# Performance work log

Measured on AMD Instinct MI355X. Metric: run time of the kernel, lower is better.

The kernel has to match this reference:

```python
import jax, jax.numpy as jnp
import numpy as np

N_NODES = 4096
N_EDGES = 131072
F_DIM = 16
H_DIM = 32

def _mlp_params(key, in_dim, hidden):
    ks = jax.random.split(key, 6)
    s1 = 1.0 / np.sqrt(in_dim); s2 = 1.0 / np.sqrt(hidden)
    return dict(
        W1=jax.random.uniform(ks[0], (in_dim, hidden), jnp.float32, -s1, s1),
        b1=jax.random.uniform(ks[1], (hidden,), jnp.float32, -s1, s1),
        W2=jax.random.uniform(ks[2], (hidden, hidden), jnp.float32, -s2, s2),
        b2=jax.random.uniform(ks[3], (hidden,), jnp.float32, -s2, s2),
        W3=jax.random.uniform(ks[4], (hidden, 1), jnp.float32, -s2, s2),
        b3=jax.random.uniform(ks[5], (1,), jnp.float32, -s2, s2),
    )

def _mlp(x, W1, b1, W2, b2, W3, b3):
    h = jax.nn.relu(x @ W1 + b1)
    h = jax.nn.relu(h @ W2 + b2)
    return (h @ W3 + b3)[..., 0]  # (E,)

def setup_inputs() -> dict:
    key = jax.random.key(0)
    k_ei, k_ef, k_s, k_p = jax.random.split(key, 4)
    edge_index = jax.random.randint(k_ei, (N_EDGES, 2), 0, N_NODES, dtype=jnp.int32)
    edge_feat = jax.random.normal(k_ef, (N_EDGES, F_DIM), dtype=jnp.float32)
    sh = _mlp_params(k_s, F_DIM, H_DIM)
    sp = _mlp_params(k_p, F_DIM, H_DIM)
    return dict(
        species_idx=0,
        edge_index=edge_index,
        edge_feat=edge_feat,
        num_nodes=N_NODES,
        sW1=sh['W1'], sb1=sh['b1'], sW2=sh['W2'], sb2=sh['b2'], sW3=sh['W3'], sb3=sh['b3'],
        pW1=sp['W1'], pb1=sp['b1'], pW2=sp['W2'], pb2=sp['b2'], pW3=sp['W3'], pb3=sp['b3'],
    )

def reference(species_idx, edge_index, edge_feat, num_nodes,
              sW1, sb1, sW2, sb2, sW3, sb3,
              pW1, pb1, pW2, pb2, pW3, pb3):
    # Edge logits: shared head + species head (species_idx selects the head;
    # here the selected head's params are passed directly).
    shared = _mlp(edge_feat, sW1, sb1, sW2, sb2, sW3, sb3)   # (E,)
    species = _mlp(edge_feat, pW1, pb1, pW2, pb2, pW3, pb3)  # (E,)
    resistance = jax.nn.softplus(shared + species) + 1e-4
    conductance = 1.0 / resistance
    i = edge_index[:, 0]
    j = edge_index[:, 1]
    # Scatter-assembled graph Laplacian (N x N)
    L = jnp.zeros((num_nodes, num_nodes), dtype=edge_feat.dtype)
    L = L.at[i, i].add(conductance)
    L = L.at[j, j].add(conductance)
    L = L.at[i, j].add(-conductance)
    L = L.at[j, i].add(-conductance)
    L_pinv = jnp.linalg.pinv(L)
    diag = jnp.diagonal(L_pinv)
    R = diag[:, None] + diag[None, :] - 2.0 * L_pinv
    return R, shared, species
```

## Files before the change

kernel.cpp:

```cpp
#include <hip/hip_runtime.h>
#include <hip/hip_bf16.h>


#define NN 4096
#define LDA 4096
#define NEDGE 131072
#define INVN (1.0f/4096.0f)

__device__ __forceinline__ float mlp_eval(const float* __restrict__ w,
                                          const float* __restrict__ x) {
  float h1[32], h2[32];
#pragma unroll
  for (int o = 0; o < 32; o += 4) {
    float4 s = *(const float4*)&w[512 + o];
#pragma unroll
    for (int i = 0; i < 16; ++i) {
      float4 wv = *(const float4*)&w[i * 32 + o];
      s.x = fmaf(x[i], wv.x, s.x); s.y = fmaf(x[i], wv.y, s.y);
      s.z = fmaf(x[i], wv.z, s.z); s.w = fmaf(x[i], wv.w, s.w);
    }
    h1[o] = fmaxf(s.x, 0.f); h1[o+1] = fmaxf(s.y, 0.f);
    h1[o+2] = fmaxf(s.z, 0.f); h1[o+3] = fmaxf(s.w, 0.f);
  }
#pragma unroll
  for (int o = 0; o < 32; o += 4) {
    float4 s = *(const float4*)&w[1568 + o];
#pragma unroll
    for (int i = 0; i < 32; ++i) {
      float4 wv = *(const float4*)&w[544 + i * 32 + o];
      s.x = fmaf(h1[i], wv.x, s.x); s.y = fmaf(h1[i], wv.y, s.y);
      s.z = fmaf(h1[i], wv.z, s.z); s.w = fmaf(h1[i], wv.w, s.w);
    }
    h2[o] = fmaxf(s.x, 0.f); h2[o+1] = fmaxf(s.y, 0.f);
    h2[o+2] = fmaxf(s.z, 0.f); h2[o+3] = fmaxf(s.w, 0.f);
  }
  float out = w[1632];
#pragma unroll
  for (int i = 0; i < 32; ++i) out = fmaf(h2[i], w[1600 + i], out);
  return out;
}

__global__ __launch_bounds__(256) void mlp_kernel(
    const float* __restrict__ ef,
    const float* __restrict__ sW1, const float* __restrict__ sb1,
    const float* __restrict__ sW2, const float* __restrict__ sb2,
    const float* __restrict__ sW3, const float* __restrict__ sb3,
    const float* __restrict__ pW1, const float* __restrict__ pb1,
    const float* __restrict__ pW2, const float* __restrict__ pb2,
    const float* __restrict__ pW3, const float* __restrict__ pb3,
    float* __restrict__ outS, float* __restrict__ outP,
    float* __restrict__ cond) {
  __shared__ float w[3328];
  int t = threadIdx.x;
  for (int i = t; i < 512; i += 256) { w[i] = sW1[i]; w[1664 + i] = pW1[i]; }
  for (int i = t; i < 1024; i += 256) { w[544 + i] = sW2[i]; w[1664 + 544 + i] = pW2[i]; }
  if (t < 32) {
    w[512 + t] = sb1[t]; w[1568 + t] = sb2[t]; w[1600 + t] = sW3[t];
    w[1664 + 512 + t] = pb1[t]; w[1664 + 1568 + t] = pb2[t]; w[1664 + 1600 + t] = pW3[t];
  }
  if (t == 0) { w[1632] = sb3[0]; w[1664 + 1632] = pb3[0]; }
  __syncthreads();
  int e = blockIdx.x * 256 + t;
  float x[16];
#pragma unroll
  for (int i = 0; i < 16; i += 4) {
    float4 v = *(const float4*)&ef[(size_t)e * 16 + i];
    x[i] = v.x; x[i+1] = v.y; x[i+2] = v.z; x[i+3] = v.w;
  }
  float s = mlp_eval(w, x);
  float p = mlp_eval(w + 1664, x);
  outS[e] = s; outP[e] = p;
  float z = s + p;
  float sp = fmaxf(z, 0.f) + log1pf(expf(-fabsf(z)));
  cond[e] = 1.0f / (sp + 1e-4f);
}

__global__ __launch_bounds__(256) void init_A(float* __restrict__ A) {
  size_t q = (size_t)blockIdx.x * 256 + threadIdx.x;
  *(float4*)&A[q * 4] = make_float4(INVN, INVN, INVN, INVN);
}

__global__ __launch_bounds__(256) void scatter_kernel(const int* __restrict__ ei,
                                                      const float* __restrict__ cond,
                                                      float* __restrict__ A) {
  int e = blockIdx.x * 256 + threadIdx.x;
  int i = ei[2 * e], j = ei[2 * e + 1];
  float c = cond[e];
  atomicAdd(&A[(size_t)i * (LDA + 1)], c);
  atomicAdd(&A[(size_t)j * (LDA + 1)], c);
  atomicAdd(&A[(size_t)i * LDA + j], -c);
  atomicAdd(&A[(size_t)j * LDA + i], -c);
}

__device__ __forceinline__ float rlane(float v, int l) {
  return __int_as_float(__builtin_amdgcn_readlane(__float_as_int(v), l));
}

__global__ __launch_bounds__(64) void potf2_wave(float* __restrict__ A, int k,
                                                 float* __restrict__ GinvAll) {
  float* blk = A + (size_t)k * 64 * (LDA + 1);
  const int lane = threadIdx.x;
  float a[64], x[64];
#pragma unroll
  for (int c = 0; c < 64; c += 4) {
    float4 v = *(const float4*)&blk[(size_t)lane * LDA + c];
    a[c] = v.x; a[c+1] = v.y; a[c+2] = v.z; a[c+3] = v.w;
    x[c]   = (c   == lane) ? 1.f : 0.f;
    x[c+1] = (c+1 == lane) ? 1.f : 0.f;
    x[c+2] = (c+2 == lane) ? 1.f : 0.f;
    x[c+3] = (c+3 == lane) ? 1.f : 0.f;
  }
#pragma unroll
  for (int j = 0; j < 64; ++j) {
    float dj = rlane(a[j], j);
    float inv = 1.0f / sqrtf(dj);
    float lij = a[j] * inv;
    a[j] = lij;
    float coefT = -lij;
    float sX = (lane == j) ? inv : 1.0f;
    float coefX = (lane > j) ? -lij : 0.0f;
#pragma unroll
    for (int c = j + 1; c < 64; ++c)
      a[c] = fmaf(coefT, rlane(lij, c), a[c]);
#pragma unroll
    for (int c = 0; c <= j; ++c) {
      float xjc = rlane(x[c], j) * inv;
      x[c] = fmaf(coefX, xjc, x[c] * sX);
    }
  }
  float* Gk = GinvAll + (size_t)k * 4096;
#pragma unroll
  for (int c = 0; c < 64; c += 4) {
    *(float4*)&blk[(size_t)lane * LDA + c] = make_float4(a[c], a[c+1], a[c+2], a[c+3]);
    *(float4*)&Gk[lane * 64 + c] = make_float4(x[c], x[c+1], x[c+2], x[c+3]);
  }
}

template <bool TA, bool TB, bool ACCUM, bool LOWER, bool KST, bool CCOMP>
__global__ __launch_bounds__(256) void gemm64(
    const float* __restrict__ Ab, long long aZ, int lda,
    const float* __restrict__ Bb, long long bZ, int ldb,
    float* __restrict__ Cb, long long cZ, int ldc, int K, float alpha) {
  int ti = blockIdx.x, tj = blockIdx.y;
  if (LOWER && tj > ti) return;
  const float* A = Ab + (long long)blockIdx.z * aZ;
  const float* B = Bb + (long long)blockIdx.z * bZ;
  __shared__ float As[16][68], Bs[16][68];
  int tid = threadIdx.x;
  int tx = tid & 15, ty = tid >> 4;
  float acc[4][4] = {};
  int m0 = ti * 64, n0 = tj * 64;
  int k0 = KST ? ti * 64 : 0;
  for (int k = k0; k < K; k += 16) {
    if (!TA) {
      int r = tid >> 2, c4 = (tid & 3) * 4;
      float4 v = *(const float4*)&A[(size_t)(m0 + r) * lda + k + c4];
      As[c4 + 0][r] = v.x; As[c4 + 1][r] = v.y; As[c4 + 2][r] = v.z; As[c4 + 3][r] = v.w;
    } else {
      int r = tid >> 4, c4 = (tid & 15) * 4;
      *(float4*)&As[r][c4] = *(const float4*)&A[(size_t)(k + r) * lda + m0 + c4];
    }
    if (TB) {
      int r = tid >> 2, c4 = (tid & 3) * 4;
      float4 v = *(const float4*)&B[(size_t)(n0 + r) * ldb + k + c4];
      Bs[c4 + 0][r] = v.x; Bs[c4 + 1][r] = v.y; Bs[c4 + 2][r] = v.z; Bs[c4 + 3][r] = v.w;
    } else {
      int r = tid >> 4, c4 = (tid & 15) * 4;
      *(float4*)&Bs[r][c4] = *(const float4*)&B[(size_t)(k + r) * ldb + n0 + c4];
    }
    __syncthreads();
#pragma unroll
    for (int kk = 0; kk < 16; ++kk) {
      float4 av = *(const float4*)&As[kk][ty * 4];
      float4 bv = *(const float4*)&Bs[kk][tx * 4];
      float a[4] = {av.x, av.y, av.z, av.w};
      float b[4] = {bv.x, bv.y, bv.z, bv.w};
#pragma unroll
      for (int i = 0; i < 4; ++i)
#pragma unroll
        for (int jj = 0; jj < 4; ++jj) acc[i][jj] = fmaf(a[i], b[jj], acc[i][jj]);
    }
    __syncthreads();
  }
  if (CCOMP) {
    float* C = Cb + ((size_t)ti * (ti + 1) / 2 + tj) * 4096;
#pragma unroll
    for (int i = 0; i < 4; ++i) {
      float4 c;
      c.x = alpha * acc[i][0]; c.y = alpha * acc[i][1];
      c.z = alpha * acc[i][2]; c.w = alpha * acc[i][3];
      *(float4*)&C[(ty * 4 + i) * 64 + tx * 4] = c;
    }
  } else {
    float* C = Cb + (long long)blockIdx.z * cZ;
#pragma unroll
    for (int i = 0; i < 4; ++i) {
      size_t off = (size_t)(m0 + ty * 4 + i) * ldc + n0 + tx * 4;
      float4 c;
      if (ACCUM) {
        c = *(float4*)&C[off];
        c.x += alpha * acc[i][0]; c.y += alpha * acc[i][1];
        c.z += alpha * acc[i][2]; c.w += alpha * acc[i][3];
      } else {
        c.x = alpha * acc[i][0]; c.y = alpha * acc[i][1];
        c.z = alpha * acc[i][2]; c.w = alpha * acc[i][3];
      }
      *(float4*)&C[off] = c;
    }
  }
}

template <bool TA, bool TB, bool ACCUM, bool TRI, bool KST, bool CCOMP>
__global__ __launch_bounds__(256) void gemm128(
    const float* __restrict__ Ab, long long aZ, int lda,
    const float* __restrict__ Bb, long long bZ, int ldb,
    float* __restrict__ Cb, long long cZ, int ldc, int K, float alpha) {
  int ti, tj;
  if (TRI) {
    int bid = blockIdx.x;
    ti = (int)((sqrtf(8.0f * bid + 1.0f) - 1.0f) * 0.5f);
    while ((ti + 1) * (ti + 2) / 2 <= bid) ++ti;
    while (ti * (ti + 1) / 2 > bid) --ti;
    tj = bid - ti * (ti + 1) / 2;
  } else {
    ti = blockIdx.x; tj = blockIdx.y;
  }
  const float* A = Ab + (long long)blockIdx.z * aZ;
  const float* B = Bb + (long long)blockIdx.z * bZ;
  __shared__ float As[16][132], Bs[16][132];
  int tid = threadIdx.x;
  int tx = tid & 15, ty = tid >> 4;
  float acc[8][8] = {};
  int m0 = ti * 128, n0 = tj * 128;
  int k0 = KST ? ti * 128 : 0;
  for (int k = k0; k < K; k += 16) {
    if (!TA) {
      int r = tid >> 1, c8 = (tid & 1) * 8;
      const float* src = &A[(size_t)(m0 + r) * lda + k + c8];
      float4 v0 = *(const float4*)src;
      float4 v1 = *(const float4*)(src + 4);
      As[c8 + 0][r] = v0.x; As[c8 + 1][r] = v0.y; As[c8 + 2][r] = v0.z; As[c8 + 3][r] = v0.w;
      As[c8 + 4][r] = v1.x; As[c8 + 5][r] = v1.y; As[c8 + 6][r] = v1.z; As[c8 + 7][r] = v1.w;
    } else {
      int r = tid >> 4, c8 = (tid & 15) * 8;
      const float* src = &A[(size_t)(k + r) * lda + m0 + c8];
      *(float4*)&As[r][c8]     = *(const float4*)src;
      *(float4*)&As[r][c8 + 4] = *(const float4*)(src + 4);
    }
    if (TB) {
      int r = tid >> 1, c8 = (tid & 1) * 8;
      const float* src = &B[(size_t)(n0 + r) * ldb + k + c8];
      float4 v0 = *(const float4*)src;
      float4 v1 = *(const float4*)(src + 4);
      Bs[c8 + 0][r] = v0.x; Bs[c8 + 1][r] = v0.y; Bs[c8 + 2][r] = v0.z; Bs[c8 + 3][r] = v0.w;
      Bs[c8 + 4][r] = v1.x; Bs[c8 + 5][r] = v1.y; Bs[c8 + 6][r] = v1.z; Bs[c8 + 7][r] = v1.w;
    } else {
      int r = tid >> 4, c8 = (tid & 15) * 8;
      const float* src = &B[(size_t)(k + r) * ldb + n0 + c8];
      *(float4*)&Bs[r][c8]     = *(const float4*)src;
      *(float4*)&Bs[r][c8 + 4] = *(const float4*)(src + 4);
    }
    __syncthreads();
#pragma unroll
    for (int kk = 0; kk < 16; ++kk) {
      float a8[8], b8[8];
      *(float4*)&a8[0] = *(const float4*)&As[kk][ty * 4];
      *(float4*)&a8[4] = *(const float4*)&As[kk][64 + ty * 4];
      *(float4*)&b8[0] = *(const float4*)&Bs[kk][tx * 4];
      *(float4*)&b8[4] = *(const float4*)&Bs[kk][64 + tx * 4];
#pragma unroll
      for (int i = 0; i < 8; ++i)
#pragma unroll
        for (int jj = 0; jj < 8; ++jj) acc[i][jj] = fmaf(a8[i], b8[jj], acc[i][jj]);
    }
    __syncthreads();
  }
  if (CCOMP) {
#pragma unroll
    for (int hr = 0; hr < 2; ++hr) {
      int TI = 2 * ti + hr;
#pragma unroll
      for (int hc = 0; hc < 2; ++hc) {
        int TJ = 2 * tj + hc;
        if (TJ > TI) continue;
        float* C = Cb + ((size_t)TI * (TI + 1) / 2 + TJ) * 4096;
#pragma unroll
        for (int i = 0; i < 4; ++i) {
          float4 c;
          c.x = alpha * acc[hr * 4 + i][hc * 4 + 0];
          c.y = alpha * acc[hr * 4 + i][hc * 4 + 1];
          c.z = alpha * acc[hr * 4 + i][hc * 4 + 2];
          c.w = alpha * acc[hr * 4 + i][hc * 4 + 3];
          *(float4*)&C[(ty * 4 + i) * 64 + tx * 4] = c;
        }
      }
    }
  } else {
    float* C = Cb + (long long)blockIdx.z * cZ;
#pragma unroll
    for (int i = 0; i < 8; ++i) {
      int row = (i < 4) ? (m0 + ty * 4 + i) : (m0 + 64 + ty * 4 + i - 4);
      float* dst0 = &C[(size_t)row * ldc + n0 + tx * 4];
      float* dst1 = dst0 + 64;
      float4 c0, c1;
      c0.x = alpha * acc[i][0]; c0.y = alpha * acc[i][1];
      c0.z = alpha * acc[i][2]; c0.w = alpha * acc[i][3];
      c1.x = alpha * acc[i][4]; c1.y = alpha * acc[i][5];
      c1.z = alpha * acc[i][6]; c1.w = alpha * acc[i][7];
      if (ACCUM) {
        float4 o0 = *(float4*)dst0, o1 = *(float4*)dst1;
        c0.x += o0.x; c0.y += o0.y; c0.z += o0.z; c0.w += o0.w;
        c1.x += o1.x; c1.y += o1.y; c1.z += o1.z; c1.w += o1.w;
      }
      *(float4*)dst0 = c0;
      *(float4*)dst1 = c1;
    }
  }
}

__global__ __launch_bounds__(256) void finish_W_prep(float* __restrict__ A,
                                                     const float* __restrict__ GinvAll) {
  size_t q = (size_t)blockIdx.x * 256 + threadIdx.x;
  int r = (int)(q >> 10), c4 = (int)(q & 1023) << 2;
  int rb = r >> 6, cb = c4 >> 6;
  if (cb == rb) {
    const float* g = GinvAll + (size_t)rb * 4096 + (size_t)(r & 63) * 64 + (c4 & 63);
    *(float4*)&A[q * 4] = *(const float4*)g;
  } else if (cb > rb) {
    *(float4*)&A[q * 4] = make_float4(0.f, 0.f, 0.f, 0.f);
  }
}

__global__ __launch_bounds__(256) void copy_diag(const float* __restrict__ Mc,
                                                 float* __restrict__ d) {
  int i = blockIdx.x * 256 + threadIdx.x;
  int tb = i >> 6;
  size_t q = (size_t)tb * (tb + 1) / 2 + tb;
  d[i] = Mc[q * 4096 + (size_t)(i & 63) * 65];
}

__global__ __launch_bounds__(256) void final_R(const float* __restrict__ Mc,
                                               const float* __restrict__ d,
                                               float* __restrict__ out) {
  size_t idx = (size_t)blockIdx.x * 256 + threadIdx.x;
  int r = (int)(idx >> 12), c = (int)(idx & 4095);
  int a = r > c ? r : c, b = r > c ? c : r;
  int ta = a >> 6, tb = b >> 6;
  size_t q = (size_t)ta * (ta + 1) / 2 + tb;
  float m = Mc[q * 4096 + (size_t)(a & 63) * 64 + (b & 63)];
  out[idx] = d[r] + d[c] - 2.0f * m;
}

extern "C" void kernel_launch(void* const* d_in, const int* in_sizes, int n_in,
                              void* d_out, int out_size, void* d_ws, size_t ws_size,
                              hipStream_t stream) {
  const int* eidx = (const int*)d_in[1];
  const float* ef = (const float*)d_in[2];
  const float* sW1 = (const float*)d_in[4],  *sb1 = (const float*)d_in[5];
  const float* sW2 = (const float*)d_in[6],  *sb2 = (const float*)d_in[7];
  const float* sW3 = (const float*)d_in[8],  *sb3 = (const float*)d_in[9];
  const float* pW1 = (const float*)d_in[10], *pb1 = (const float*)d_in[11];
  const float* pW2 = (const float*)d_in[12], *pb2 = (const float*)d_in[13];
  const float* pW3 = (const float*)d_in[14], *pb3 = (const float*)d_in[15];

  float* dout = (float*)d_out;
  float* dA = dout;
  float* outS = dout + (size_t)NN * NN;
  float* outP = outS + NEDGE;

  float* ws = (float*)d_ws;
  float* Mc = ws;
  float* U = ws + 8519680ull;
  float* cond = U;
  float* Ginv = U;
  float* Tbuf = U;
  float* diagb = U;

  mlp_kernel<<<NEDGE / 256, 256, 0, stream>>>(ef, sW1, sb1, sW2, sb2, sW3, sb3,
                                              pW1, pb1, pW2, pb2, pW3, pb3,
                                              outS, outP, cond);
  init_A<<<(NN * NN / 4) / 256, 256, 0, stream>>>(dA);
  scatter_kernel<<<NEDGE / 256, 256, 0, stream>>>(eidx, cond, dA);

  for (int p = 0; p < 16; ++p) {
    int ct = p * 4;
    for (int kk = 0; kk < 4; ++kk) {
      int k = ct + kk;
      potf2_wave<<<1, 64, 0, stream>>>(dA, k, Ginv);
      int rem = NN - (k + 1) * 64;
      if (rem > 0) {
        float* panel = dA + (size_t)(k + 1) * 64 * LDA + (size_t)k * 64;
        gemm64<false, true, false, false, false, false>
            <<<dim3(rem / 64, 1, 1), 256, 0, stream>>>(
                panel, 0, LDA, Ginv + (size_t)k * 4096, 0, 64, panel, 0, LDA,
                64, 1.0f);
        int pcols = 3 - kk;
        if (pcols > 0) {
          float* trail = dA + (size_t)(k + 1) * 64 * (LDA + 1);
          gemm64<false, true, true, true, false, false>
              <<<dim3(rem / 64, pcols, 1), 256, 0, stream>>>(
                  panel, 0, LDA, panel, 0, LDA, trail, 0, LDA, 64, -1.0f);
        }
      }
    }
    int c0 = p * 256;
    int rem2 = NN - c0 - 256;
    if (rem2 > 0) {
      float* Lp = dA + (size_t)(c0 + 256) * LDA + c0;
      float* trail = dA + (size_t)(c0 + 256) * (LDA + 1);
      int nt = rem2 / 128;
      gemm128<false, true, true, true, false, false>
          <<<dim3(nt * (nt + 1) / 2, 1, 1), 256, 0, stream>>>(
              Lp, 0, LDA, Lp, 0, LDA, trail, 0, LDA, 256, -1.0f);
    }
  }

  finish_W_prep<<<(NN * NN / 4) / 256, 256, 0, stream>>>(dA, Ginv);

  for (int S = 64; S <= 2048; S *= 2) {
    int np = NN / (2 * S);
    long long pz = (long long)2 * S * (LDA + 1);
    if (S == 64) {
      gemm64<false, false, false, false, false, false>
          <<<dim3(1, 1, np), 256, 0, stream>>>(
              dA + (size_t)S * LDA, pz, LDA, dA, pz, LDA,
              Tbuf, (long long)S * S, S, S, 1.0f);
      gemm64<false, false, false, false, false, false>
          <<<dim3(1, 1, np), 256, 0, stream>>>(
              dA + (size_t)S * (LDA + 1), pz, LDA, Tbuf, (long long)S * S, S,
              dA + (size_t)S * LDA, pz, LDA, S, -1.0f);
    } else {
      gemm128<false, false, false, false, false, false>
          <<<dim3(S / 128, S / 128, np), 256, 0, stream>>>(
              dA + (size_t)S * LDA, pz, LDA, dA, pz, LDA,
              Tbuf, (long long)S * S, S, S, 1.0f);
      gemm128<false, false, false, false, false, false>
          <<<dim3(S / 128, S / 128, np), 256, 0, stream>>>(
              dA + (size_t)S * (LDA + 1), pz, LDA, Tbuf, (long long)S * S, S,
              dA + (size_t)S * LDA, pz, LDA, S, -1.0f);
    }
  }

  gemm128<true, false, false, true, true, true>
      <<<dim3(528, 1, 1), 256, 0, stream>>>(dA, 0, LDA, dA, 0, LDA, Mc, 0, 64,
                                            NN, 1.0f);

  copy_diag<<<NN / 256, 256, 0, stream>>>(Mc, diagb);
  final_R<<<(NN * NN) / 256, 256, 0, stream>>>(Mc, diagb, dout);
}
```

Measured before the change: 5.171 ms.

## Fuse 256-wide diagonal Cholesky into one kernel, add fused panel TRSM and K-split Gram GEMM

Replaces the per-64-column sequence of potf2, panel GEMM and small SYRK launches with a single 512-thread kernel that factors each 256x256 diagonal block in shared memory. A new trsm_panel256 kernel then solves the whole 256-wide panel per 64-row block. The final triangular Gram GEMM is split along K into two halves that accumulate with atomics into a zeroed workspace, which doubles parallelism for the imbalanced KST launch. The aim is to cut the many tiny serial launches on the critical path, at the cost of running diagonal work on a single block and paying for atomic accumulation.

```diff
diff --git a/kernel.cpp b/kernel.cpp
--- a/kernel.cpp
+++ b/kernel.cpp
@@ -80,6 +80,11 @@
   *(float4*)&A[q * 4] = make_float4(INVN, INVN, INVN, INVN);
 }
 
+__global__ __launch_bounds__(256) void zero_ws(float* __restrict__ P) {
+  size_t q = (size_t)blockIdx.x * 256 + threadIdx.x;
+  *(float4*)&P[q * 4] = make_float4(0.f, 0.f, 0.f, 0.f);
+}
+
 __global__ __launch_bounds__(256) void scatter_kernel(const int* __restrict__ ei,
                                                       const float* __restrict__ cond,
                                                       float* __restrict__ A) {
@@ -96,10 +101,9 @@
   return __int_as_float(__builtin_amdgcn_readlane(__float_as_int(v), l));
 }
 
-__global__ __launch_bounds__(64) void potf2_wave(float* __restrict__ A, int k,
-                                                 float* __restrict__ GinvAll) {
-  float* blk = A + (size_t)k * 64 * (LDA + 1);
-  const int lane = threadIdx.x;
+__device__ __noinline__ void potf2_dev(float* __restrict__ A, int kt, int lane,
+                                       float (* __restrict__ GT)[68]) {
+  float* blk = A + (size_t)kt * 64 * (LDA + 1);
   float a[64], x[64];
 #pragma unroll
   for (int c = 0; c < 64; c += 4) {
@@ -128,11 +132,206 @@
       x[c] = fmaf(coefX, xjc, x[c] * sX);
     }
   }
-  float* Gk = GinvAll + (size_t)k * 4096;
-#pragma unroll
-  for (int c = 0; c < 64; c += 4) {
+#pragma unroll
+  for (int c = 0; c < 64; c += 4)
     *(float4*)&blk[(size_t)lane * LDA + c] = make_float4(a[c], a[c+1], a[c+2], a[c+3]);
-    *(float4*)&Gk[lane * 64 + c] = make_float4(x[c], x[c+1], x[c+2], x[c+3]);
+#pragma unroll
+  for (int c = 0; c < 64; ++c) GT[c][lane] = x[c];
+}
+
+__device__ __forceinline__ void syrk_tile(float* __restrict__ A, int t0, int ti_, int tj_,
+                                          const float (* __restrict__ LtA)[68],
+                                          const float (* __restrict__ LtB)[68], int gtid) {
+  int tx = gtid & 15, ty = gtid >> 4;
+  float acc[4][4] = {};
+  for (int k = 0; k < 64; ++k) {
+    float4 a4 = *(const float4*)&LtA[k][ty * 4];
+    float4 b4 = *(const float4*)&LtB[k][tx * 4];
+    float aa[4] = {a4.x, a4.y, a4.z, a4.w};
+    float bb[4] = {b4.x, b4.y, b4.z, b4.w};
+#pragma unroll
+    for (int i = 0; i < 4; ++i)
+#pragma unroll
+      for (int jj = 0; jj < 4; ++jj) acc[i][jj] = fmaf(aa[i], bb[jj], acc[i][jj]);
+  }
+  float* C = A + ((size_t)(t0 + ti_) * 64) * LDA + (size_t)(t0 + tj_) * 64;
+#pragma unroll
+  for (int i = 0; i < 4; ++i) {
+    float* p = &C[(size_t)(ty * 4 + i) * LDA + tx * 4];
+    float4 c = *(float4*)p;
+    c.x -= acc[i][0]; c.y -= acc[i][1]; c.z -= acc[i][2]; c.w -= acc[i][3];
+    *(float4*)p = c;
+  }
+}
+
+__global__ __launch_bounds__(512) void potrf_diag256(float* __restrict__ A,
+                                                     float* __restrict__ GinvAll,
+                                                     int p) {
+  __shared__ float GT[64][68];
+  __shared__ float At[2][64][68];
+  __shared__ float Lt[3][64][68];
+  int tid = threadIdx.x;
+  int wid = tid >> 6, lane = tid & 63;
+  int grp = tid >> 8, gtid = tid & 255;
+  int t0 = p * 4;
+  for (int kk = 0; kk < 4; ++kk) {
+    if (wid == 0) {
+      potf2_dev(A, t0 + kk, lane, GT);
+    } else if (grp == 1) {
+      const int TI_[5] = {2, 3, 2, 3, 3};
+      const int TJ_[5] = {1, 1, 2, 2, 3};
+#pragma unroll 5
+      for (int t = 0; t < 5; ++t) {
+        bool on = (kk == 1) || (kk == 2 && t >= 3);
+        if (on)
+          syrk_tile(A, t0, TI_[t], TJ_[t], Lt[TI_[t] - kk], Lt[TJ_[t] - kk], gtid);
+      }
+    }
+    __syncthreads();
+    {
+      int base = (t0 + kk) * 4096;
+#pragma unroll 8
+      for (int u = 0; u < 8; ++u) {
+        int q = tid * 8 + u;
+        GinvAll[base + q] = GT[q & 63][q >> 6];
+      }
+    }
+    for (int rnd = 0; rnd < 2; ++rnd) {
+      int it = kk + 1 + rnd * 2 + grp;
+      bool act = (it <= 3);
+      if (act) {
+        for (int q = gtid; q < 1024; q += 256) {
+          int r = q >> 4, k4 = (q & 15) << 2;
+          float4 v = *(const float4*)&A[((size_t)(t0 + it) * 64 + r) * LDA +
+                                        (size_t)(t0 + kk) * 64 + k4];
+          At[grp][k4 + 0][r] = v.x; At[grp][k4 + 1][r] = v.y;
+          At[grp][k4 + 2][r] = v.z; At[grp][k4 + 3][r] = v.w;
+        }
+      }
+      __syncthreads();
+      if (act) {
+        int tx = gtid & 15, ty = gtid >> 4;
+        float acc[4][4] = {};
+        for (int k = 0; k < 64; ++k) {
+          float4 a4 = *(const float4*)&At[grp][k][ty * 4];
+          float4 b4 = *(const float4*)&GT[k][tx * 4];
+          float aa[4] = {a4.x, a4.y, a4.z, a4.w};
+          float bb[4] = {b4.x, b4.y, b4.z, b4.w};
+#pragma unroll
+          for (int i = 0; i < 4; ++i)
+#pragma unroll
+            for (int jj = 0; jj < 4; ++jj) acc[i][jj] = fmaf(aa[i], bb[jj], acc[i][jj]);
+        }
+        int s = it - kk - 1;
+#pragma unroll
+        for (int jj = 0; jj < 4; ++jj)
+          *(float4*)&Lt[s][tx * 4 + jj][ty * 4] =
+              make_float4(acc[0][jj], acc[1][jj], acc[2][jj], acc[3][jj]);
+        float* C = A + ((size_t)(t0 + it) * 64) * LDA + (size_t)(t0 + kk) * 64;
+#pragma unroll
+        for (int i = 0; i < 4; ++i)
+          *(float4*)&C[(size_t)(ty * 4 + i) * LDA + tx * 4] =
+              make_float4(acc[i][0], acc[i][1], acc[i][2], acc[i][3]);
+      }
+      __syncthreads();
+    }
+    if (kk < 3 && grp == 0)
+      syrk_tile(A, t0, kk + 1, kk + 1, Lt[0], Lt[0], gtid);
+    __syncthreads();
+  }
+}
+
+__global__ __launch_bounds__(256) void trsm_panel256(float* __restrict__ A,
+                                                     const float* __restrict__ GinvAll,
+                                                     int p) {
+  __shared__ float Sr[64][260];
+  __shared__ float Bt[64][68];
+  int tid = threadIdx.x;
+  int c0 = p * 256;
+  int r0 = c0 + 256 + blockIdx.x * 64;
+  for (int q = tid; q < 4096; q += 256) {
+    int r = q >> 6, c4 = (q & 63) << 2;
+    *(float4*)&Sr[r][c4] = *(const float4*)&A[(size_t)(r0 + r) * LDA + c0 + c4];
+  }
+  __syncthreads();
+  int tx = tid & 15, ty = tid >> 4;
+  for (int j = 0; j < 4; ++j) {
+    float acc2[4][4] = {};
+    for (int p2 = 0; p2 < j; ++p2) {
+      for (int q = tid; q < 1024; q += 256) {
+        int c = q >> 4, k4 = (q & 15) << 2;
+        float4 v = *(const float4*)&A[(size_t)(c0 + j * 64 + c) * LDA +
+                                      c0 + p2 * 64 + k4];
+        Bt[k4 + 0][c] = v.x; Bt[k4 + 1][c] = v.y;
+        Bt[k4 + 2][c] = v.z; Bt[k4 + 3][c] = v.w;
+      }
+      __syncthreads();
+      for (int k = 0; k < 64; ++k) {
+        float a0 = Sr[ty * 4 + 0][p2 * 64 + k];
+        float a1 = Sr[ty * 4 + 1][p2 * 64 + k];
+        float a2 = Sr[ty * 4 + 2][p2 * 64 + k];
+        float a3 = Sr[ty * 4 + 3][p2 * 64 + k];
+        float4 b = *(const float4*)&Bt[k][tx * 4];
+        acc2[0][0] = fmaf(a0, b.x, acc2[0][0]); acc2[0][1] = fmaf(a0, b.y, acc2[0][1]);
+        acc2[0][2] = fmaf(a0, b.z, acc2[0][2]); acc2[0][3] = fmaf(a0, b.w, acc2[0][3]);
+        acc2[1][0] = fmaf(a1, b.x, acc2[1][0]); acc2[1][1] = fmaf(a1, b.y, acc2[1][1]);
+        acc2[1][2] = fmaf(a1, b.z, acc2[1][2]); acc2[1][3] = fmaf(a1, b.w, acc2[1][3]);
+        acc2[2][0] = fmaf(a2, b.x, acc2[2][0]); acc2[2][1] = fmaf(a2, b.y, acc2[2][1]);
+        acc2[2][2] = fmaf(a2, b.z, acc2[2][2]); acc2[2][3] = fmaf(a2, b.w, acc2[2][3]);
+        acc2[3][0] = fmaf(a3, b.x, acc2[3][0]); acc2[3][1] = fmaf(a3, b.y, acc2[3][1]);
+        acc2[3][2] = fmaf(a3, b.z, acc2[3][2]); acc2[3][3] = fmaf(a3, b.w, acc2[3][3]);
+      }
+      __syncthreads();
+    }
+    if (j > 0) {
+#pragma unroll
+      for (int i = 0; i < 4; ++i) {
+        Sr[ty * 4 + i][j * 64 + tx * 4 + 0] -= acc2[i][0];
+        Sr[ty * 4 + i][j * 64 + tx * 4 + 1] -= acc2[i][1];
+        Sr[ty * 4 + i][j * 64 + tx * 4 + 2] -= acc2[i][2];
+        Sr[ty * 4 + i][j * 64 + tx * 4 + 3] -= acc2[i][3];
+      }
+    }
+    __syncthreads();
+    {
+      const float* G = GinvAll + (size_t)(p * 4 + j) * 4096;
+      for (int q = tid; q < 1024; q += 256) {
+        int c = q >> 4, k4 = (q & 15) << 2;
+        float4 v = *(const float4*)&G[c * 64 + k4];
+        Bt[k4 + 0][c] = v.x; Bt[k4 + 1][c] = v.y;
+        Bt[k4 + 2][c] = v.z; Bt[k4 + 3][c] = v.w;
+      }
+    }
+    __syncthreads();
+    float acc3[4][4] = {};
+    for (int k = 0; k < 64; ++k) {
+      float a0 = Sr[ty * 4 + 0][j * 64 + k];
+      float a1 = Sr[ty * 4 + 1][j * 64 + k];
+      float a2 = Sr[ty * 4 + 2][j * 64 + k];
+      float a3 = Sr[ty * 4 + 3][j * 64 + k];
+      float4 b = *(const float4*)&Bt[k][tx * 4];
+      acc3[0][0] = fmaf(a0, b.x, acc3[0][0]); acc3[0][1] = fmaf(a0, b.y, acc3[0][1]);
+      acc3[0][2] = fmaf(a0, b.z, acc3[0][2]); acc3[0][3] = fmaf(a0, b.w, acc3[0][3]);
+      acc3[1][0] = fmaf(a1, b.x, acc3[1][0]); acc3[1][1] = fmaf(a1, b.y, acc3[1][1]);
+      acc3[1][2] = fmaf(a1, b.z, acc3[1][2]); acc3[1][3] = fmaf(a1, b.w, acc3[1][3]);
+      acc3[2][0] = fmaf(a2, b.x, acc3[2][0]); acc3[2][1] = fmaf(a2, b.y, acc3[2][1]);
+      acc3[2][2] = fmaf(a2, b.z, acc3[2][2]); acc3[2][3] = fmaf(a2, b.w, acc3[2][3]);
+      acc3[3][0] = fmaf(a3, b.x, acc3[3][0]); acc3[3][1] = fmaf(a3, b.y, acc3[3][1]);
+      acc3[3][2] = fmaf(a3, b.z, acc3[3][2]); acc3[3][3] = fmaf(a3, b.w, acc3[3][3]);
+    }
+    __syncthreads();
+#pragma unroll
+    for (int i = 0; i < 4; ++i) {
+      Sr[ty * 4 + i][j * 64 + tx * 4 + 0] = acc3[i][0];
+      Sr[ty * 4 + i][j * 64 + tx * 4 + 1] = acc3[i][1];
+      Sr[ty * 4 + i][j * 64 + tx * 4 + 2] = acc3[i][2];
+      Sr[ty * 4 + i][j * 64 + tx * 4 + 3] = acc3[i][3];
+    }
+    __syncthreads();
+  }
+  for (int q = tid; q < 4096; q += 256) {
+    int r = q >> 6, c4 = (q & 63) << 2;
+    *(float4*)&A[(size_t)(r0 + r) * LDA + c0 + c4] = *(float4*)&Sr[r][c4];
   }
 }
 
@@ -182,35 +381,25 @@
     }
     __syncthreads();
   }
-  if (CCOMP) {
-    float* C = Cb + ((size_t)ti * (ti + 1) / 2 + tj) * 4096;
-#pragma unroll
-    for (int i = 0; i < 4; ++i) {
-      float4 c;
+  float* C = Cb + (long long)blockIdx.z * cZ;
+#pragma unroll
+  for (int i = 0; i < 4; ++i) {
+    size_t off = (size_t)(m0 + ty * 4 + i) * ldc + n0 + tx * 4;
+    float4 c;
+    if (ACCUM) {
+      c = *(float4*)&C[off];
+      c.x += alpha * acc[i][0]; c.y += alpha * acc[i][1];
+      c.z += alpha * acc[i][2]; c.w += alpha * acc[i][3];
+    } else {
       c.x = alpha * acc[i][0]; c.y = alpha * acc[i][1];
       c.z = alpha * acc[i][2]; c.w = alpha * acc[i][3];
-      *(float4*)&C[(ty * 4 + i) * 64 + tx * 4] = c;
-    }
-  } else {
-    float* C = Cb + (long long)blockIdx.z * cZ;
-#pragma unroll
-    for (int i = 0; i < 4; ++i) {
-      size_t off = (size_t)(m0 + ty * 4 + i) * ldc + n0 + tx * 4;
-      float4 c;
-      if (ACCUM) {
-        c = *(float4*)&C[off];
-        c.x += alpha * acc[i][0]; c.y += alpha * acc[i][1];
-        c.z += alpha * acc[i][2]; c.w += alpha * acc[i][3];
-      } else {
-        c.x = alpha * acc[i][0]; c.y = alpha * acc[i][1];
-        c.z = alpha * acc[i][2]; c.w = alpha * acc[i][3];
-      }
-      *(float4*)&C[off] = c;
-    }
-  }
-}
-
-template <bool TA, bool TB, bool ACCUM, bool TRI, bool KST, bool CCOMP>
+    }
+    *(float4*)&C[off] = c;
+  }
+}
+
+template <bool TA, bool TB, bool ACCUM, bool TRI, bool KST, bool CCOMP,
+          bool ATOMIC, bool KSPLIT>
 __global__ __launch_bounds__(256) void gemm128(
     const float* __restrict__ Ab, long long aZ, int lda,
     const float* __restrict__ Bb, long long bZ, int ldb,
@@ -225,15 +414,20 @@
   } else {
     ti = blockIdx.x; tj = blockIdx.y;
   }
-  const float* A = Ab + (long long)blockIdx.z * aZ;
-  const float* B = Bb + (long long)blockIdx.z * bZ;
+  int k0 = KST ? ti * 128 : 0;
+  int kEnd = K;
+  if (KSPLIT) {
+    if (blockIdx.z == 0) { kEnd = 2048; if (k0 >= kEnd) return; }
+    else { k0 = (k0 > 2048) ? k0 : 2048; }
+  }
+  const float* A = KSPLIT ? Ab : Ab + (long long)blockIdx.z * aZ;
+  const float* B = KSPLIT ? Bb : Bb + (long long)blockIdx.z * bZ;
   __shared__ float As[16][132], Bs[16][132];
   int tid = threadIdx.x;
   int tx = tid & 15, ty = tid >> 4;
   float acc[8][8] = {};
   int m0 = ti * 128, n0 = tj * 128;
-  int k0 = KST ? ti * 128 : 0;
-  for (int k = k0; k < K; k += 16) {
+  for (int k = k0; k < kEnd; k += 16) {
     if (!TA) {
       int r = tid >> 1, c8 = (tid & 1) * 8;
       const float* src = &A[(size_t)(m0 + r) * lda + k + c8];
@@ -286,12 +480,20 @@
         float* C = Cb + ((size_t)TI * (TI + 1) / 2 + TJ) * 4096;
 #pragma unroll
         for (int i = 0; i < 4; ++i) {
-          float4 c;
-          c.x = alpha * acc[hr * 4 + i][hc * 4 + 0];
-          c.y = alpha * acc[hr * 4 + i][hc * 4 + 1];
-          c.z = alpha * acc[hr * 4 + i][hc * 4 + 2];
-          c.w = alpha * acc[hr * 4 + i][hc * 4 + 3];
-          *(float4*)&C[(ty * 4 + i) * 64 + tx * 4] = c;
+          if (ATOMIC) {
+            float* pbase = &C[(ty * 4 + i) * 64 + tx * 4];
+            atomicAdd(pbase + 0, alpha * acc[hr * 4 + i][hc * 4 + 0]);
+            atomicAdd(pbase + 1, alpha * acc[hr * 4 + i][hc * 4 + 1]);
+            atomicAdd(pbase + 2, alpha * acc[hr * 4 + i][hc * 4 + 2]);
+            atomicAdd(pbase + 3, alpha * acc[hr * 4 + i][hc * 4 + 3]);
+          } else {
+            float4 c;
+            c.x = alpha * acc[hr * 4 + i][hc * 4 + 0];
+            c.y = alpha * acc[hr * 4 + i][hc * 4 + 1];
+            c.z = alpha * acc[hr * 4 + i][hc * 4 + 2];
+            c.w = alpha * acc[hr * 4 + i][hc * 4 + 3];
+            *(float4*)&C[(ty * 4 + i) * 64 + tx * 4] = c;
+          }
         }
       }
     }
@@ -379,37 +581,19 @@
   mlp_kernel<<<NEDGE / 256, 256, 0, stream>>>(ef, sW1, sb1, sW2, sb2, sW3, sb3,
                                               pW1, pb1, pW2, pb2, pW3, pb3,
                                               outS, outP, cond);
+  zero_ws<<<2080, 256, 0, stream>>>(Mc);
   init_A<<<(NN * NN / 4) / 256, 256, 0, stream>>>(dA);
   scatter_kernel<<<NEDGE / 256, 256, 0, stream>>>(eidx, cond, dA);
 
   for (int p = 0; p < 16; ++p) {
-    int ct = p * 4;
-    for (int kk = 0; kk < 4; ++kk) {
-      int k = ct + kk;
-      potf2_wave<<<1, 64, 0, stream>>>(dA, k, Ginv);
-      int rem = NN - (k + 1) * 64;
-      if (rem > 0) {
-        float* panel = dA + (size_t)(k + 1) * 64 * LDA + (size_t)k * 64;
-        gemm64<false, true, false, false, false, false>
-            <<<dim3(rem / 64, 1, 1), 256, 0, stream>>>(
-                panel, 0, LDA, Ginv + (size_t)k * 4096, 0, 64, panel, 0, LDA,
-                64, 1.0f);
-        int pcols = 3 - kk;
-        if (pcols > 0) {
-          float* trail = dA + (size_t)(k + 1) * 64 * (LDA + 1);
-          gemm64<false, true, true, true, false, false>
-              <<<dim3(rem / 64, pcols, 1), 256, 0, stream>>>(
-                  panel, 0, LDA, panel, 0, LDA, trail, 0, LDA, 64, -1.0f);
-        }
-      }
-    }
-    int c0 = p * 256;
-    int rem2 = NN - c0 - 256;
-    if (rem2 > 0) {
-      float* Lp = dA + (size_t)(c0 + 256) * LDA + c0;
-      float* trail = dA + (size_t)(c0 + 256) * (LDA + 1);
-      int nt = rem2 / 128;
-      gemm128<false, true, true, true, false, false>
+    potrf_diag256<<<1, 512, 0, stream>>>(dA, Ginv, p);
+    int rem = NN - (p + 1) * 256;
+    if (rem > 0) {
+      trsm_panel256<<<rem / 64, 256, 0, stream>>>(dA, Ginv, p);
+      int nt = rem / 128;
+      float* Lp = dA + (size_t)((p + 1) * 256) * LDA + (size_t)p * 256;
+      float* trail = dA + (size_t)((p + 1) * 256) * (LDA + 1);
+      gemm128<false, true, true, true, false, false, false, false>
           <<<dim3(nt * (nt + 1) / 2, 1, 1), 256, 0, stream>>>(
               Lp, 0, LDA, Lp, 0, LDA, trail, 0, LDA, 256, -1.0f);
     }
@@ -430,19 +614,19 @@
               dA + (size_t)S * (LDA + 1), pz, LDA, Tbuf, (long long)S * S, S,
               dA + (size_t)S * LDA, pz, LDA, S, -1.0f);
     } else {
-      gemm128<false, false, false, false, false, false>
+      gemm128<false, false, false, false, false, false, false, false>
           <<<dim3(S / 128, S / 128, np), 256, 0, stream>>>(
               dA + (size_t)S * LDA, pz, LDA, dA, pz, LDA,
               Tbuf, (long long)S * S, S, S, 1.0f);
-      gemm128<false, false, false, false, false, false>
+      gemm128<false, false, false, false, false, false, false, false>
           <<<dim3(S / 128, S / 128, np), 256, 0, stream>>>(
               dA + (size_t)S * (LDA + 1), pz, LDA, Tbuf, (long long)S * S, S,
               dA + (size_t)S * LDA, pz, LDA, S, -1.0f);
     }
   }
 
-  gemm128<true, false, false, true, true, true>
-      <<<dim3(528, 1, 1), 256, 0, stream>>>(dA, 0, LDA, dA, 0, LDA, Mc, 0, 64,
+  gemm128<true, false, false, true, true, true, true, true>
+      <<<dim3(528, 1, 2), 256, 0, stream>>>(dA, 0, LDA, dA, 0, LDA, Mc, 0, 64,
                                             NN, 1.0f);
 
   copy_diag<<<NN / 256, 256, 0, stream>>>(Mc, diagb);
```

New measurement: 5.583 ms. 1.08x slower.
